# Optimization experiments

Measured on AMD Instinct MI355X. Metric: run time of the kernel, lower is better.

## Reference

```python
import jax, jax.numpy as jnp
import numpy as np

# Regular (3,6) rate-1/2 LDPC Tanner graph
N = 8192        # variable nodes (codeword length n)
R = 4096        # check nodes (r = n - k)
DV = 3          # variable-node degree
DC = 6          # check-node degree
E = N * DV      # number of edges (= R * DC)
B = 1024        # batch of codewords decoded simultaneously
ITERS = 10      # fixed BP iterations (max_iterations; early-exit dropped for jit)
CLIP = 0.999    # original clips the tanh-product to (-0.999, 0.999)


def setup_inputs() -> dict:
    rng = np.random.default_rng(0)
    # Edge list of a regular bipartite graph: each var appears DV times,
    # each check appears DC times; random socket permutation (Gallager style).
    edge_var = np.repeat(np.arange(N, dtype=np.int32), DV)
    edge_check = rng.permutation(np.repeat(np.arange(R, dtype=np.int32), DC))
    key = jax.random.key(0)
    received = jax.random.normal(key, (B, N), dtype=jnp.float32)
    return {
        "received": received,
        "edge_var": jnp.asarray(edge_var),
        "edge_check": jnp.asarray(edge_check),
    }


def reference(received, edge_var, edge_check):
    """Batched sum-product (belief propagation) LDPC decoding.

    received: [B, N] soft channel values; noise_variance = 1.0.
    Messages live on edges, shape [E, B].
    """
    noise_variance = 1.0
    llr = 2.0 * received / noise_variance            # [B, N] channel LLRs
    llr_t = llr.T                                     # [N, B]

    v2c0 = llr_t[edge_var]                            # [E, B] initial var->check msgs
    c2v0 = jnp.zeros_like(v2c0)                       # [E, B] initial check->var msgs

    def body(i, carry):
        v2c, _ = carry
        # --- check-node update: leave-one-out product of tanh(msg/2) ---
        t = jnp.tanh(0.5 * v2c)                       # [E, B]
        prod_c = jax.ops.segment_prod(t, edge_check, num_segments=R)  # [R, B]
        loo = prod_c[edge_check] / t                  # leave-one-out product, [E, B]
        c2v = 2.0 * jnp.arctanh(jnp.clip(loo, -CLIP, CLIP))
        # --- variable-node update: leave-one-out sum of check msgs + channel ---
        tot = llr_t + jax.ops.segment_sum(c2v, edge_var, num_segments=N)  # [N, B]
        v2c_new = tot[edge_var] - c2v                 # [E, B]
        return (v2c_new, c2v)

    _, c2v = jax.lax.fori_loop(0, ITERS, body, (v2c0, c2v0))

    # Final posterior LLRs: channel LLR + sum of incoming check->var msgs
    final_llrs = llr + jax.ops.segment_sum(c2v, edge_var, num_segments=N).T  # [B, N]
    decoded_bits = (final_llrs < 0).astype(jnp.int32)
    return final_llrs, decoded_bits
```

## Files before the change

kernel.cpp:

```cpp
#include <hip/hip_runtime.h>


#define N_  8192
#define R_  4096
#define DV_ 3
#define DC_ 6
#define E_  (N_ * DV_)
#define B_  1024
#define ITERS_ 10

#define THREADS_ 1024
#define CPT_ (R_ / THREADS_)
#define VPT_ (N_ / THREADS_)

#define LOG2E_ 1.442695041f
#define LN2_   0.69314718f

__global__ __launch_bounds__(256) void build_edges_kernel(
    const int* __restrict__ edge_check, int* __restrict__ counters,
    int* __restrict__ check_edges) {
  int e = blockIdx.x * 256 + threadIdx.x;
  if (e < E_) {
    int r = edge_check[e];
    int s = atomicAdd(&counters[r], 1);
    check_edges[r * DC_ + s] = e;
  }
}

__global__ __launch_bounds__(256) void sort_edges_kernel(
    int* __restrict__ check_edges) {
  int r = blockIdx.x * 256 + threadIdx.x;
  if (r >= R_) return;
  int e0 = check_edges[r * DC_ + 0], e1 = check_edges[r * DC_ + 1];
  int e2 = check_edges[r * DC_ + 2], e3 = check_edges[r * DC_ + 3];
  int e4 = check_edges[r * DC_ + 4], e5 = check_edges[r * DC_ + 5];
#define CSWAP(a, b) { int lo = min(a, b), hi = max(a, b); a = lo; b = hi; }
  CSWAP(e0, e5) CSWAP(e1, e3) CSWAP(e2, e4)
  CSWAP(e1, e2) CSWAP(e3, e4)
  CSWAP(e0, e3) CSWAP(e2, e5)
  CSWAP(e0, e1) CSWAP(e2, e3) CSWAP(e4, e5)
  CSWAP(e1, e2) CSWAP(e3, e4)
#undef CSWAP
  check_edges[r * DC_ + 0] = e0; check_edges[r * DC_ + 1] = e1;
  check_edges[r * DC_ + 2] = e2; check_edges[r * DC_ + 3] = e3;
  check_edges[r * DC_ + 4] = e4; check_edges[r * DC_ + 5] = e5;
}

__global__ __launch_bounds__(THREADS_) void persistent_kernel(
    const float* __restrict__ recv, const int* __restrict__ check_edges,
    float* __restrict__ out) {
  __shared__ float q_s[E_];
  __shared__ float E_s[N_];
  const int b = blockIdx.x;
  const int tid = threadIdx.x;
  const float* r = recv + (size_t)b * N_;

  int eidx[CPT_][DC_];
  int vidx[CPT_][DC_];
#pragma unroll
  for (int c = 0; c < CPT_; c++) {
    int rr = c * THREADS_ + tid;
#pragma unroll
    for (int i = 0; i < DC_; i++) {
      int e = check_edges[rr * DC_ + i];
      eidx[c][i] = e;
      vidx[c][i] = (int)((unsigned)e / 3u);
    }
  }
  float hn[CPT_][DC_], hd[CPT_][DC_];
#pragma unroll
  for (int c = 0; c < CPT_; c++)
#pragma unroll
    for (int i = 0; i < DC_; i++) { hn[c][i] = 1.0f; hd[c][i] = 1.0f; }

  float e_llr[VPT_];
#pragma unroll
  for (int k = 0; k < VPT_; k++) {
    float llr = 2.0f * r[tid + k * THREADS_];
    e_llr[k] = __builtin_amdgcn_exp2f(llr * LOG2E_);
    E_s[tid + k * THREADS_] = e_llr[k];
  }
  __syncthreads();

  for (int iter = 0; iter < ITERS_; iter++) {
#pragma unroll
    for (int c = 0; c < CPT_; c++) {
      float t[DC_];
#pragma unroll
      for (int i = 0; i < DC_; i++) {
        float A = E_s[vidx[c][i]] * hn[c][i];
        float num = A - hd[c][i];
        float den = A + hd[c][i];
        t[i] = num * __builtin_amdgcn_rcpf(den);
      }
      float loo[DC_];
      float run = 1.0f;
#pragma unroll
      for (int i = 0; i < DC_; i++) { loo[i] = run; run *= t[i]; }
      run = 1.0f;
#pragma unroll
      for (int i = DC_ - 1; i >= 0; i--) { loo[i] *= run; run *= t[i]; }
#pragma unroll
      for (int i = 0; i < DC_; i++) {
        float y = loo[i];
        y = fminf(fmaxf(y, -0.999f), 0.999f);
        float qd = 1.0f - y;
        float qn = 1.0f + y;
        q_s[eidx[c][i]] = qn * __builtin_amdgcn_rcpf(qd);
        hn[c][i] = qd;
        hd[c][i] = qn;
      }
    }
    __syncthreads();
#pragma unroll
    for (int k = 0; k < VPT_; k++) {
      int v = tid + k * THREADS_;
      E_s[v] = ((e_llr[k] * q_s[3 * v]) * q_s[3 * v + 1]) * q_s[3 * v + 2];
    }
    __syncthreads();
  }

  const size_t BN = (size_t)B_ * N_;
#pragma unroll
  for (int k = 0; k < VPT_; k++) {
    int n = tid + k * THREADS_;
    float val = LN2_ * __builtin_amdgcn_logf(E_s[n]);
    out[(size_t)b * N_ + n] = val;
    out[BN + (size_t)b * N_ + n] = (val < 0.0f) ? 1.0f : 0.0f;
  }
}

extern "C" void kernel_launch(void* const* d_in, const int* in_sizes, int n_in,
                              void* d_out, int out_size, void* d_ws,
                              size_t ws_size, hipStream_t stream) {
  const float* recv = (const float*)d_in[0];
  const int* edge_check = (const int*)d_in[2];
  float* out = (float*)d_out;

  char* ws = (char*)d_ws;
  size_t off = 0;
  int* counters = (int*)(ws + off);    off += (size_t)R_ * sizeof(int);
  int* check_edges = (int*)(ws + off); off += (size_t)R_ * DC_ * sizeof(int);

  hipMemsetAsync(counters, 0, (size_t)R_ * sizeof(int), stream);
  build_edges_kernel<<<(E_ + 255) / 256, 256, 0, stream>>>(edge_check, counters,
                                                           check_edges);
  sort_edges_kernel<<<(R_ + 255) / 256, 256, 0, stream>>>(check_edges);
  persistent_kernel<<<B_, THREADS_, 0, stream>>>(recv, check_edges, out);
}
```

Measured before the change: 246.6 us.

## Build sorted check-edge lists with ballot scan, vectorize variable-node q loads

Replaces the memset plus atomic scatter plus sorting-network kernels with a single kernel in which each check node's wavefront scans the whole edge list and uses ballot and popcount to write its edges in ascending order. This removes two launches and the memset. Each of the 4096 blocks now reads the full 24K-entry edge array, which adds redundant global and L2 traffic. The variable-node update also loads the first two q values as a single float2 from shared memory; with odd v that address is only 4-byte aligned.

Measured after the change: 338.5 us. 37.3% more time.

```diff
diff --git a/kernel.cpp b/kernel.cpp
--- a/kernel.cpp
+++ b/kernel.cpp
@@ -16,34 +16,21 @@
 #define LOG2E_ 1.442695041f
 #define LN2_   0.69314718f
 
-__global__ __launch_bounds__(256) void build_edges_kernel(
-    const int* __restrict__ edge_check, int* __restrict__ counters,
-    int* __restrict__ check_edges) {
-  int e = blockIdx.x * 256 + threadIdx.x;
-  if (e < E_) {
-    int r = edge_check[e];
-    int s = atomicAdd(&counters[r], 1);
-    check_edges[r * DC_ + s] = e;
+__global__ __launch_bounds__(64) void build_edges_kernel(
+    const int* __restrict__ edge_check, int* __restrict__ check_edges) {
+  int r = blockIdx.x;
+  int lane = threadIdx.x;
+  int slot = 0;
+  for (int base = 0; base < E_; base += 64) {
+    int e = base + lane;
+    bool m = (edge_check[e] == r);
+    unsigned long long mask = __ballot(m);
+    if (m) {
+      int my = slot + __popcll(mask & ((1ULL << lane) - 1ULL));
+      check_edges[r * DC_ + my] = e;
+    }
+    slot += __popcll(mask);
   }
-}
-
-__global__ __launch_bounds__(256) void sort_edges_kernel(
-    int* __restrict__ check_edges) {
-  int r = blockIdx.x * 256 + threadIdx.x;
-  if (r >= R_) return;
-  int e0 = check_edges[r * DC_ + 0], e1 = check_edges[r * DC_ + 1];
-  int e2 = check_edges[r * DC_ + 2], e3 = check_edges[r * DC_ + 3];
-  int e4 = check_edges[r * DC_ + 4], e5 = check_edges[r * DC_ + 5];
-#define CSWAP(a, b) { int lo = min(a, b), hi = max(a, b); a = lo; b = hi; }
-  CSWAP(e0, e5) CSWAP(e1, e3) CSWAP(e2, e4)
-  CSWAP(e1, e2) CSWAP(e3, e4)
-  CSWAP(e0, e3) CSWAP(e2, e5)
-  CSWAP(e0, e1) CSWAP(e2, e3) CSWAP(e4, e5)
-  CSWAP(e1, e2) CSWAP(e3, e4)
-#undef CSWAP
-  check_edges[r * DC_ + 0] = e0; check_edges[r * DC_ + 1] = e1;
-  check_edges[r * DC_ + 2] = e2; check_edges[r * DC_ + 3] = e3;
-  check_edges[r * DC_ + 4] = e4; check_edges[r * DC_ + 5] = e5;
 }
 
 __global__ __launch_bounds__(THREADS_) void persistent_kernel(
@@ -115,7 +102,10 @@
 #pragma unroll
     for (int k = 0; k < VPT_; k++) {
       int v = tid + k * THREADS_;
-      E_s[v] = ((e_llr[k] * q_s[3 * v]) * q_s[3 * v + 1]) * q_s[3 * v + 2];
+      float2 q01;
+      __builtin_memcpy(&q01, &q_s[3 * v], sizeof(float2));
+      float q2 = q_s[3 * v + 2];
+      E_s[v] = ((e_llr[k] * q01.x) * q01.y) * q2;
     }
     __syncthreads();
   }
@@ -138,13 +128,8 @@
   float* out = (float*)d_out;
 
   char* ws = (char*)d_ws;
-  size_t off = 0;
-  int* counters = (int*)(ws + off);    off += (size_t)R_ * sizeof(int);
-  int* check_edges = (int*)(ws + off); off += (size_t)R_ * DC_ * sizeof(int);
+  int* check_edges = (int*)ws;
 
-  hipMemsetAsync(counters, 0, (size_t)R_ * sizeof(int), stream);
-  build_edges_kernel<<<(E_ + 255) / 256, 256, 0, stream>>>(edge_check, counters,
-                                                           check_edges);
-  sort_edges_kernel<<<(R_ + 255) / 256, 256, 0, stream>>>(check_edges);
+  build_edges_kernel<<<R_, 64, 0, stream>>>(edge_check, check_edges);
   persistent_kernel<<<B_, THREADS_, 0, stream>>>(recv, check_edges, out);
 }
```
